# Optimization experiments

Measured on AMD Instinct MI355X. Metric: run time of the kernel, lower is better.

The kernel has to match this reference:

```python
import jax, jax.numpy as jnp
import numpy as np

N_NODES = 100000
N_EDGES = 3200000
VM, VA, PG, QG, PD, QD = 0, 1, 2, 3, 4, 5
G, B = 0, 1


def setup_inputs() -> dict:
    key = jax.random.key(0)
    k1, k2, k3, k4, k5 = jax.random.split(key, 5)
    pred = jax.random.normal(k1, (N_NODES, 6), dtype=jnp.float32)
    target = jax.random.normal(k2, (N_NODES, 6), dtype=jnp.float32)
    edge_index = jax.random.randint(k3, (2, N_EDGES), 0, N_NODES, dtype=jnp.int64)
    edge_attr = jax.random.normal(k4, (N_EDGES, 2), dtype=jnp.float32)
    mask = jax.random.randint(k5, (N_NODES, 6), 0, 2) == 1
    return {"pred": pred, "target": target, "edge_index": edge_index,
            "edge_attr": edge_attr, "mask": mask}


def reference(pred, target, edge_index, edge_attr, mask):
    # temp_pred[~mask] = target[~mask]
    temp_pred = jnp.where(mask, pred, target)
    vm = temp_pred[:, VM]
    va = temp_pred[:, VA]
    pg = temp_pred[:, PG]
    qg = temp_pred[:, QG]
    pd = temp_pred[:, PD]
    qd = temp_pred[:, QD]
    g = edge_attr[:, G]
    b = edge_attr[:, B]
    src, dst = edge_index[0], edge_index[1]

    v_from = vm[src]                      # [E] gather
    v_to = vm[dst]
    ang = va[src] - va[dst]
    c, s = jnp.cos(ang), jnp.sin(ang)
    vv = v_from * v_to
    p_flow = vv * (g * c + b * s)         # [E]
    q_flow = vv * (g * s - b * c)

    # scatter-add flows into source nodes
    p_calc = jax.ops.segment_sum(p_flow, src, num_segments=N_NODES)
    q_calc = jax.ops.segment_sum(q_flow, src, num_segments=N_NODES)

    p_imb = pg - pd - p_calc
    q_imb = qg - qd - q_calc
    loss = jnp.mean(p_imb ** 2) + jnp.mean(q_imb ** 2)
    return loss
```

## Files before the change

### kernel.cpp

```cpp
#include <hip/hip_runtime.h>
#include <cstdint>

#define N_NODES 100000
#define N_EDGES 3200000
#define SPAN    256
#define SHIFT   8
#define NB      ((N_NODES + SPAN - 1) / SPAN)
#define CHUNK   4096
#define BTHREADS 512
#define NITER   (CHUNK / BTHREADS)
#define NBLK_A  ((N_EDGES + CHUNK - 1) / CHUNK)
#define K_MAX   12288

#define FP_SCALE 4096.0f
#define FP_INV   (1.0f / 4096.0f)

__global__ __launch_bounds__(256)
void prep_kernel(const float* __restrict__ pred,
                 const float* __restrict__ target,
                 const void* __restrict__ mask,
                 float2* __restrict__ u_tab,
                 float2* __restrict__ base_pq,
                 unsigned long long* __restrict__ ovf,
                 uint32_t* __restrict__ gcursor,
                 float* __restrict__ d_out, int out_size) {
    __shared__ int s_mask8;
    if (threadIdx.x < 64) {
        uint32_t w = ((const uint32_t*)mask)[threadIdx.x];
        bool nz = (w & 0xFFFFFF00u) != 0u;
        unsigned long long m = __ballot(nz);
        if (threadIdx.x == 0) s_mask8 = (m != 0ull) ? 1 : 0;
    }
    if (blockIdx.x == 0) {
        for (int b = threadIdx.x; b < NB; b += 256) gcursor[b] = 0u;
        if (threadIdx.x == 0)
            for (int k = 0; k < out_size; ++k) d_out[k] = 0.0f;
    }
    __syncthreads();

    int i = blockIdx.x * 256 + threadIdx.x;
    if (i >= N_NODES) return;

    const float2* p2 = (const float2*)pred;
    const float2* t2 = (const float2*)target;
    float2 pa = p2[3 * i], pb = p2[3 * i + 1], pc = p2[3 * i + 2];
    float2 ta = t2[3 * i], tb = t2[3 * i + 1], tc = t2[3 * i + 2];
    float pr[6] = {pa.x, pa.y, pb.x, pb.y, pc.x, pc.y};
    float tg[6] = {ta.x, ta.y, tb.x, tb.y, tc.x, tc.y};
    int mk[6];
    if (s_mask8) {
        const uint16_t* mu = (const uint16_t*)mask;
        uint16_t m0 = mu[3 * i], m1 = mu[3 * i + 1], m2 = mu[3 * i + 2];
        mk[0] = m0 & 0xFF; mk[1] = m0 >> 8;
        mk[2] = m1 & 0xFF; mk[3] = m1 >> 8;
        mk[4] = m2 & 0xFF; mk[5] = m2 >> 8;
    } else {
        const int2* mi = (const int2*)mask;
        int2 m0 = mi[3 * i], m1 = mi[3 * i + 1], m2 = mi[3 * i + 2];
        mk[0] = m0.x; mk[1] = m0.y; mk[2] = m1.x;
        mk[3] = m1.y; mk[4] = m2.x; mk[5] = m2.y;
    }
    float tp[6];
    #pragma unroll
    for (int j = 0; j < 6; ++j) tp[j] = mk[j] ? pr[j] : tg[j];

    float s, c;
    sincosf(tp[1], &s, &c);
    u_tab[i]   = make_float2(tp[0] * c, tp[0] * s);
    base_pq[i] = make_float2(tp[2] - tp[4], tp[3] - tp[5]);
    ovf[i] = 0ull;
}

__global__ __launch_bounds__(BTHREADS)
void bin_kernel(const void* __restrict__ edge_index,
                const float2* __restrict__ edge_attr,
                const float2* __restrict__ u_tab,
                uint32_t* __restrict__ gcursor,
                uint2* __restrict__ recs,
                unsigned long long* __restrict__ ovf,
                int k_cap) {
    __shared__ uint2 s_rec[CHUNK];
    __shared__ uint32_t s_cnt[NB];
    __shared__ uint32_t s_pref[NB + 1];
    __shared__ uint32_t s_gbase[NB];
    __shared__ uint32_t s_wsum[8], s_woff[8];
    __shared__ int s_i64;

    const int tid = threadIdx.x;
    const int lane = tid & 63, wid = tid >> 6;
    if (tid < 64) {
        uint32_t w = ((const uint32_t*)edge_index)[tid];
        bool nz = (tid & 1) && (w != 0u);
        unsigned long long m = __ballot(nz);
        if (tid == 0) s_i64 = (m == 0ull) ? 1 : 0;
    }
    if (tid < NB) s_cnt[tid] = 0u;
    __syncthreads();
    const bool is64 = (s_i64 != 0);
    const int ebase = blockIdx.x * CHUNK;
    const int nE = min(CHUNK, N_EDGES - ebase);

    uint32_t src_r[NITER];
    #pragma unroll
    for (int it = 0; it < NITER; ++it) {
        int j = it * BTHREADS + tid;
        uint32_t s = 0u;
        if (j < nE) {
            int e = ebase + j;
            s = is64 ? (uint32_t)((const unsigned long long*)edge_index)[e]
                     : ((const uint32_t*)edge_index)[e];
            atomicAdd(&s_cnt[s >> SHIFT], 1u);
        }
        src_r[it] = s;
    }
    __syncthreads();

    {
        uint32_t v0 = (tid < NB) ? s_cnt[tid] : 0u;
        uint32_t x = v0;
        #pragma unroll
        for (int off = 1; off < 64; off <<= 1) {
            uint32_t y = (uint32_t)__shfl_up((int)x, off, 64);
            if (lane >= off) x += y;
        }
        if (lane == 63) s_wsum[wid] = x;
        __syncthreads();
        if (tid < 8) {
            uint32_t w0 = s_wsum[tid];
            uint32_t xx = w0;
            #pragma unroll
            for (int off = 1; off < 8; off <<= 1) {
                uint32_t y = (uint32_t)__shfl_up((int)xx, off, 64);
                if (tid >= off) xx += y;
            }
            s_woff[tid] = xx - w0;
        }
        __syncthreads();
        uint32_t incl = x + s_woff[wid];
        if (tid < NB) s_pref[tid + 1] = incl;
        if (tid == 0) s_pref[0] = 0u;
        if (tid < NB) {
            uint32_t excl = incl - v0;
            s_gbase[tid] = v0 ? atomicAdd(&gcursor[tid], v0) : 0u;
            s_cnt[tid] = 0u;
            (void)excl;
        }
        __syncthreads();
    }

    #pragma unroll
    for (int it = 0; it < NITER; ++it) {
        int j = it * BTHREADS + tid;
        if (j < nE) {
            int e = ebase + j;
            uint32_t dst = is64
                ? (uint32_t)((const unsigned long long*)edge_index)[(size_t)N_EDGES + e]
                : ((const uint32_t*)edge_index)[(size_t)N_EDGES + e];
            float2 gb = edge_attr[e];
            float2 u  = u_tab[dst];
            float vr = gb.x * u.x - gb.y * u.y;
            float vi = -(gb.y * u.x + gb.x * u.y);
            uint32_t nid = src_r[it];
            uint32_t bk = nid >> SHIFT, lid = nid & (SPAN - 1);
            uint32_t r = atomicAdd(&s_cnt[bk], 1u);
            uint2 rc;
            rc.x = (__float_as_uint(vr) & ~0xFFu) | lid;
            rc.y = (__float_as_uint(vi) & ~0x1FFu) | bk;
            s_rec[s_pref[bk] + r] = rc;
        }
    }
    __syncthreads();

    for (int slot = tid; slot < nE; slot += BTHREADS) {
        uint2 rc = s_rec[slot];
        uint32_t bk = rc.y & 0x1FFu;
        uint32_t pos = s_gbase[bk] + ((uint32_t)slot - s_pref[bk]);
        if ((int)pos < k_cap) {
            recs[(size_t)bk * k_cap + pos] = rc;
        } else {
            float vr = __uint_as_float(rc.x & ~0xFFu);
            float vi = __uint_as_float(rc.y & ~0x1FFu);
            uint32_t nid = (bk << SHIFT) | (rc.x & 0xFFu);
            int pi = __float2int_rn(vr * FP_SCALE);
            int qi = __float2int_rn(vi * FP_SCALE);
            unsigned long long enc =
                ((unsigned long long)(long long)pi << 32) +
                (unsigned long long)(unsigned int)qi;
            atomicAdd(&ovf[nid], enc);
        }
    }
}

__global__ __launch_bounds__(1024)
void reduce_kernel(const uint2* __restrict__ recs,
                   const uint32_t* __restrict__ gcursor,
                   const float2* __restrict__ u_tab,
                   const float2* __restrict__ base_pq,
                   const unsigned long long* __restrict__ ovf,
                   float* __restrict__ d_out, int k_cap) {
    __shared__ float2 s_acc[4][SPAN];
    __shared__ float s_part[16];
    if (threadIdx.x < SPAN) {
        #pragma unroll
        for (int r = 0; r < 4; ++r) s_acc[r][threadIdx.x] = make_float2(0.0f, 0.0f);
    }
    __syncthreads();

    const int b = blockIdx.x;
    const int n = min((int)gcursor[b], k_cap);
    const int rep = (threadIdx.x >> 6) & 3;
    const uint2* r = recs + (size_t)b * k_cap;
    for (int j = threadIdx.x; j < n; j += 1024) {
        uint2 rc = r[j];
        uint32_t lid = rc.x & 0xFFu;
        atomicAdd(&s_acc[rep][lid].x, __uint_as_float(rc.x & ~0xFFu));
        atomicAdd(&s_acc[rep][lid].y, __uint_as_float(rc.y & ~0x1FFu));
    }
    __syncthreads();

    float v = 0.0f;
    int node = b * SPAN + (int)threadIdx.x;
    if (threadIdx.x < SPAN && node < N_NODES) {
        float2 S = make_float2(0.0f, 0.0f);
        #pragma unroll
        for (int rr = 0; rr < 4; ++rr) {
            float2 t = s_acc[rr][threadIdx.x];
            S.x += t.x; S.y += t.y;
        }
        unsigned long long u = ovf[node];
        if (u) {
            int qs = (int)(unsigned int)(u & 0xFFFFFFFFull);
            long long rem = (long long)(u - (unsigned long long)(long long)qs);
            int ps = (int)(rem >> 32);
            S.x += (float)ps * FP_INV;
            S.y += (float)qs * FP_INV;
        }
        float2 ui = u_tab[node];
        float2 bp = base_pq[node];
        float pc = ui.x * S.x - ui.y * S.y;
        float qc = ui.x * S.y + ui.y * S.x;
        float p = bp.x - pc, q = bp.y - qc;
        v = p * p + q * q;
    }
    #pragma unroll
    for (int off = 32; off > 0; off >>= 1) v += __shfl_down(v, off, 64);
    if ((threadIdx.x & 63) == 0) s_part[threadIdx.x >> 6] = v;
    __syncthreads();
    if (threadIdx.x == 0) {
        float t = 0.0f;
        #pragma unroll
        for (int w = 0; w < 16; ++w) t += s_part[w];
        atomicAdd(d_out, t * (1.0f / (float)N_NODES));
    }
}

extern "C" void kernel_launch(void* const* d_in, const int* in_sizes, int n_in,
                              void* d_out, int out_size, void* d_ws, size_t ws_size,
                              hipStream_t stream) {
    const float*  pred       = (const float*)d_in[0];
    const float*  target     = (const float*)d_in[1];
    const void*   edge_index = d_in[2];
    const float2* edge_attr  = (const float2*)d_in[3];
    const void*   mask       = d_in[4];
    float* out = (float*)d_out;

    char* ws = (char*)d_ws;
    float2*             u_tab   = (float2*)ws;
    float2*             base_pq = (float2*)(ws + 800000);
    unsigned long long* ovf     = (unsigned long long*)(ws + 1600000);
    uint32_t*           gcursor = (uint32_t*)(ws + 2400000);
    uint2*              recs    = (uint2*)(ws + 2404096);

    long long avail = (long long)ws_size - 2404096;
    long long kc = (avail > 0) ? (avail / ((long long)NB * 8)) : 0;
    int k_cap = (int)((kc > K_MAX) ? K_MAX : kc);

    prep_kernel<<<(N_NODES + 255) / 256, 256, 0, stream>>>(
        pred, target, mask, u_tab, base_pq, ovf, gcursor, out, out_size);

    bin_kernel<<<NBLK_A, BTHREADS, 0, stream>>>(
        edge_index, edge_attr, u_tab, gcursor, recs, ovf, k_cap);

    reduce_kernel<<<NB, 1024, 0, stream>>>(
        recs, gcursor, u_tab, base_pq, ovf, out, k_cap);
}
```

Before: 198.5 us.

## Write per-block sorted chunks contiguously and let reduce walk per-block prefix tables

The bin kernel no longer reserves global per-bucket slots with atomics. It now writes its locally bucket-sorted chunk contiguously with 16-byte stores and also stores its prefix table. Each reduce block then has one thread per edge chunk (782) read that chunk's segment for its bucket. This removes the gcursor atomics, the scattered record writes and the fixed-point overflow path. The cost is that reduce reads are now serial per thread, over about 4 records each, from scattered locations, and reading the prefix table adds traffic.

```diff
diff --git a/kernel.cpp b/kernel.cpp
--- a/kernel.cpp
+++ b/kernel.cpp
@@ -7,13 +7,10 @@
 #define SHIFT   8
 #define NB      ((N_NODES + SPAN - 1) / SPAN)
 #define CHUNK   4096
-#define BTHREADS 512
-#define NITER   (CHUNK / BTHREADS)
-#define NBLK_A  ((N_EDGES + CHUNK - 1) / CHUNK)
-#define K_MAX   12288
-
-#define FP_SCALE 4096.0f
-#define FP_INV   (1.0f / 4096.0f)
+#define BTH     512
+#define NITER   (CHUNK / BTH)
+#define NBLK    ((N_EDGES + CHUNK - 1) / CHUNK)
+#define PREF_W  (NB + 1)
 
 __global__ __launch_bounds__(256)
 void prep_kernel(const float* __restrict__ pred,
@@ -21,8 +18,6 @@
                  const void* __restrict__ mask,
                  float2* __restrict__ u_tab,
                  float2* __restrict__ base_pq,
-                 unsigned long long* __restrict__ ovf,
-                 uint32_t* __restrict__ gcursor,
                  float* __restrict__ d_out, int out_size) {
     __shared__ int s_mask8;
     if (threadIdx.x < 64) {
@@ -31,11 +26,8 @@
         unsigned long long m = __ballot(nz);
         if (threadIdx.x == 0) s_mask8 = (m != 0ull) ? 1 : 0;
     }
-    if (blockIdx.x == 0) {
-        for (int b = threadIdx.x; b < NB; b += 256) gcursor[b] = 0u;
-        if (threadIdx.x == 0)
-            for (int k = 0; k < out_size; ++k) d_out[k] = 0.0f;
-    }
+    if (blockIdx.x == 0 && threadIdx.x == 0)
+        for (int k = 0; k < out_size; ++k) d_out[k] = 0.0f;
     __syncthreads();
 
     int i = blockIdx.x * 256 + threadIdx.x;
@@ -68,21 +60,17 @@
     sincosf(tp[1], &s, &c);
     u_tab[i]   = make_float2(tp[0] * c, tp[0] * s);
     base_pq[i] = make_float2(tp[2] - tp[4], tp[3] - tp[5]);
-    ovf[i] = 0ull;
-}
-
-__global__ __launch_bounds__(BTHREADS)
+}
+
+__global__ __launch_bounds__(BTH)
 void bin_kernel(const void* __restrict__ edge_index,
                 const float2* __restrict__ edge_attr,
                 const float2* __restrict__ u_tab,
-                uint32_t* __restrict__ gcursor,
                 uint2* __restrict__ recs,
-                unsigned long long* __restrict__ ovf,
-                int k_cap) {
+                uint32_t* __restrict__ pref) {
     __shared__ uint2 s_rec[CHUNK];
     __shared__ uint32_t s_cnt[NB];
-    __shared__ uint32_t s_pref[NB + 1];
-    __shared__ uint32_t s_gbase[NB];
+    __shared__ uint32_t s_pref[PREF_W];
     __shared__ uint32_t s_wsum[8], s_woff[8];
     __shared__ int s_i64;
 
@@ -103,7 +91,7 @@
     uint32_t src_r[NITER];
     #pragma unroll
     for (int it = 0; it < NITER; ++it) {
-        int j = it * BTHREADS + tid;
+        int j = it * BTH + tid;
         uint32_t s = 0u;
         if (j < nE) {
             int e = ebase + j;
@@ -139,18 +127,13 @@
         uint32_t incl = x + s_woff[wid];
         if (tid < NB) s_pref[tid + 1] = incl;
         if (tid == 0) s_pref[0] = 0u;
-        if (tid < NB) {
-            uint32_t excl = incl - v0;
-            s_gbase[tid] = v0 ? atomicAdd(&gcursor[tid], v0) : 0u;
-            s_cnt[tid] = 0u;
-            (void)excl;
-        }
+        if (tid < NB) s_cnt[tid] = 0u;
         __syncthreads();
     }
 
     #pragma unroll
     for (int it = 0; it < NITER; ++it) {
-        int j = it * BTHREADS + tid;
+        int j = it * BTH + tid;
         if (j < nE) {
             int e = ebase + j;
             uint32_t dst = is64
@@ -165,39 +148,29 @@
             uint32_t r = atomicAdd(&s_cnt[bk], 1u);
             uint2 rc;
             rc.x = (__float_as_uint(vr) & ~0xFFu) | lid;
-            rc.y = (__float_as_uint(vi) & ~0x1FFu) | bk;
+            rc.y = __float_as_uint(vi);
             s_rec[s_pref[bk] + r] = rc;
         }
     }
     __syncthreads();
 
-    for (int slot = tid; slot < nE; slot += BTHREADS) {
-        uint2 rc = s_rec[slot];
-        uint32_t bk = rc.y & 0x1FFu;
-        uint32_t pos = s_gbase[bk] + ((uint32_t)slot - s_pref[bk]);
-        if ((int)pos < k_cap) {
-            recs[(size_t)bk * k_cap + pos] = rc;
-        } else {
-            float vr = __uint_as_float(rc.x & ~0xFFu);
-            float vi = __uint_as_float(rc.y & ~0x1FFu);
-            uint32_t nid = (bk << SHIFT) | (rc.x & 0xFFu);
-            int pi = __float2int_rn(vr * FP_SCALE);
-            int qi = __float2int_rn(vi * FP_SCALE);
-            unsigned long long enc =
-                ((unsigned long long)(long long)pi << 32) +
-                (unsigned long long)(unsigned int)qi;
-            atomicAdd(&ovf[nid], enc);
-        }
-    }
+    {
+        const uint4* s4 = (const uint4*)s_rec;
+        uint4* a4 = (uint4*)(recs + (size_t)blockIdx.x * CHUNK);
+        for (int k = tid; k < nE / 2; k += BTH) a4[k] = s4[k];
+        if ((nE & 1) && tid == 0)
+            recs[(size_t)blockIdx.x * CHUNK + nE - 1] = s_rec[nE - 1];
+    }
+    for (int b = tid; b < PREF_W; b += BTH)
+        pref[(size_t)blockIdx.x * PREF_W + b] = s_pref[b];
 }
 
 __global__ __launch_bounds__(1024)
 void reduce_kernel(const uint2* __restrict__ recs,
-                   const uint32_t* __restrict__ gcursor,
+                   const uint32_t* __restrict__ pref,
                    const float2* __restrict__ u_tab,
                    const float2* __restrict__ base_pq,
-                   const unsigned long long* __restrict__ ovf,
-                   float* __restrict__ d_out, int k_cap) {
+                   float* __restrict__ d_out) {
     __shared__ float2 s_acc[4][SPAN];
     __shared__ float s_part[16];
     if (threadIdx.x < SPAN) {
@@ -207,14 +180,17 @@
     __syncthreads();
 
     const int b = blockIdx.x;
-    const int n = min((int)gcursor[b], k_cap);
     const int rep = (threadIdx.x >> 6) & 3;
-    const uint2* r = recs + (size_t)b * k_cap;
-    for (int j = threadIdx.x; j < n; j += 1024) {
-        uint2 rc = r[j];
-        uint32_t lid = rc.x & 0xFFu;
-        atomicAdd(&s_acc[rep][lid].x, __uint_as_float(rc.x & ~0xFFu));
-        atomicAdd(&s_acc[rep][lid].y, __uint_as_float(rc.y & ~0x1FFu));
+    if (threadIdx.x < NBLK) {
+        const uint32_t* prow = pref + (size_t)threadIdx.x * PREF_W;
+        uint32_t s = prow[b], e = prow[b + 1];
+        const uint2* arena = recs + (size_t)threadIdx.x * CHUNK;
+        for (uint32_t j = s; j < e; ++j) {
+            uint2 rc = arena[j];
+            uint32_t lid = rc.x & 0xFFu;
+            atomicAdd(&s_acc[rep][lid].x, __uint_as_float(rc.x & ~0xFFu));
+            atomicAdd(&s_acc[rep][lid].y, __uint_as_float(rc.y));
+        }
     }
     __syncthreads();
 
@@ -226,14 +202,6 @@
         for (int rr = 0; rr < 4; ++rr) {
             float2 t = s_acc[rr][threadIdx.x];
             S.x += t.x; S.y += t.y;
-        }
-        unsigned long long u = ovf[node];
-        if (u) {
-            int qs = (int)(unsigned int)(u & 0xFFFFFFFFull);
-            long long rem = (long long)(u - (unsigned long long)(long long)qs);
-            int ps = (int)(rem >> 32);
-            S.x += (float)ps * FP_INV;
-            S.y += (float)qs * FP_INV;
         }
         float2 ui = u_tab[node];
         float2 bp = base_pq[node];
@@ -265,22 +233,17 @@
     float* out = (float*)d_out;
 
     char* ws = (char*)d_ws;
-    float2*             u_tab   = (float2*)ws;
-    float2*             base_pq = (float2*)(ws + 800000);
-    unsigned long long* ovf     = (unsigned long long*)(ws + 1600000);
-    uint32_t*           gcursor = (uint32_t*)(ws + 2400000);
-    uint2*              recs    = (uint2*)(ws + 2404096);
-
-    long long avail = (long long)ws_size - 2404096;
-    long long kc = (avail > 0) ? (avail / ((long long)NB * 8)) : 0;
-    int k_cap = (int)((kc > K_MAX) ? K_MAX : kc);
+    float2*   u_tab   = (float2*)ws;
+    float2*   base_pq = (float2*)(ws + 800000);
+    uint32_t* pref    = (uint32_t*)(ws + 1600000);
+    uint2*    recs    = (uint2*)(ws + 2826176);
 
     prep_kernel<<<(N_NODES + 255) / 256, 256, 0, stream>>>(
-        pred, target, mask, u_tab, base_pq, ovf, gcursor, out, out_size);
-
-    bin_kernel<<<NBLK_A, BTHREADS, 0, stream>>>(
-        edge_index, edge_attr, u_tab, gcursor, recs, ovf, k_cap);
+        pred, target, mask, u_tab, base_pq, out, out_size);
+
+    bin_kernel<<<NBLK, BTH, 0, stream>>>(
+        edge_index, edge_attr, u_tab, recs, pref);
 
     reduce_kernel<<<NB, 1024, 0, stream>>>(
-        recs, gcursor, u_tab, base_pq, ovf, out, k_cap);
-}
+        recs, pref, u_tab, base_pq, out);
+}
```

Result: faster. 173.2 us (-12.7%).
